# Optimization experiments

Measured on AMD Instinct MI355X. Metric: run time of the kernel, lower is better.

## Reference

```python
import jax, jax.numpy as jnp
import numpy as np

B, T, K = 64, 4096, 48  # batch, seq_len, n_tags


def setup_inputs() -> dict:
    key = jax.random.key(0)
    k1, k2, k3 = jax.random.split(key, 3)
    labels = jax.random.randint(k1, (B, T), 0, K)
    y_true = jax.nn.one_hot(labels, K, dtype=jnp.float32)  # one-hot targets, per dense_loss docstring
    y_pred = jax.random.normal(k2, (B, T, K), dtype=jnp.float32)  # emission scores
    trans = jax.random.normal(k3, (K, K), dtype=jnp.float32) * 0.1  # transition matrix (glorot-ish scale)
    return {"y_true": y_true, "y_pred": y_pred, "trans": trans}


def reference(y_true, y_pred, trans):
    # mask: positions where all emission scores > -1e6 (padding marker)
    mask = jnp.all(y_pred > -1e6, axis=2, keepdims=True).astype(y_pred.dtype)  # (B,T,1)
    y_true = y_true * mask
    y_pred = y_pred * mask

    # target_score: per-label emission score + transition score of the true path
    point_score = jnp.einsum('bni,bni->b', y_true, y_pred)
    trans_score = jnp.einsum('bni,ij,bnj->b', y_true[:, :-1], trans, y_true[:, 1:])
    target = point_score + trans_score  # (B,)

    # log_norm_step recurrence (CRF forward algorithm), fused as a single scan
    init = y_pred[:, 0]  # (B,K)
    xs = jnp.swapaxes(y_pred[:, 1:], 0, 1)  # (T-1,B,K)
    ms = jnp.swapaxes(mask[:, 1:], 0, 1)    # (T-1,B,1)

    def step(s, xm):
        x, m = xm
        # logsumexp over previous-tag axis: s (B,K_prev) + trans (K_prev,K_cur)
        new = jax.scipy.special.logsumexp(s[:, :, None] + trans[None, :, :], axis=1) + x
        s = m * new + (1.0 - m) * s
        return s, None

    s_final, _ = jax.lax.scan(step, init, (xs, ms))
    log_norm = jax.scipy.special.logsumexp(s_final, axis=1)  # (B,)

    # dense_loss returns log_norm - target_score (negative log-likelihood per example)
    return log_norm - target
```

## Files before the change

kernel.cpp:

```cpp
#include <hip/hip_runtime.h>

#define BB 64
#define TT 4096
#define KK 48
#define UST 56
#define PST 56
#define WS_LS_OFF 16384
#define WS_U_OFF 32768
#define SEGBYTES 6144

typedef __bf16 bf16_t;
typedef bf16_t bf16x8 __attribute__((ext_vector_type(8)));
typedef float f32x4 __attribute__((ext_vector_type(4)));
typedef float f32x16 __attribute__((ext_vector_type(16)));

__device__ __forceinline__ float fexp(float x) {
    return __builtin_amdgcn_exp2f(x * 1.4426950408889634f);
}
__device__ __forceinline__ float flog2(float x) { return __builtin_amdgcn_logf(x); }
__device__ __forceinline__ float rdlanef(float v, int l) {
    return __int_as_float(__builtin_amdgcn_readlane(__float_as_int(v), l));
}
__device__ __forceinline__ unsigned int bf16bits(float f) {
    return (unsigned int)__builtin_bit_cast(unsigned short, (bf16_t)f);
}
__device__ __forceinline__ float bf2f(bf16_t h) {
    return __uint_as_float(((unsigned int)__builtin_bit_cast(unsigned short, h)) << 16);
}
__device__ __forceinline__ unsigned int pktrunc(float lo, float hi) {
    return __builtin_amdgcn_perm(__float_as_uint(hi), __float_as_uint(lo), 0x07060302u);
}

__global__ __launch_bounds__(256) void fused_kernel(
    const float* __restrict__ y_true, const float* __restrict__ y_pred,
    const float* __restrict__ trans, float* __restrict__ ws_target,
    int* __restrict__ ws_ls, bf16_t* __restrict__ ws_u, int nseg) {
    const int s = blockIdx.x, b = blockIdx.y;
    const int seglen = TT / nseg;
    const int nch = seglen / 64;
    const int tid = threadIdx.x;
    const int w = tid >> 6;
    const int lane = tid & 63;
    const int q = lane >> 4;
    const int n = lane & 15;
    const int ncol = 16 * w + n;

    __shared__ __align__(16) float4 exf[64 * 13];
    __shared__ __align__(16) bf16_t Ubuf[48 * UST + 16];
    __shared__ unsigned long long pb;
    __shared__ int lsb[4];

    bf16x8 afrag[3][2];
    if (w < 3) {
#pragma unroll
        for (int mt = 0; mt < 3; mt++) {
#pragma unroll
            for (int ks = 0; ks < 2; ks++) {
                bf16x8 f;
#pragma unroll
                for (int j = 0; j < 8; j++) {
                    int k = 32 * ks + 8 * q + j;
                    float v = (k < KK) ? fexp(trans[k * KK + 16 * mt + n]) : 0.0f;
                    f[j] = (bf16_t)v;
                }
                afrag[mt][ks] = f;
            }
        }
    }

    {
        uint4* p = (uint4*)Ubuf;
        for (int i = tid; i < (48 * UST + 16) / 8; i += 256) p[i] = make_uint4(0, 0, 0, 0);
    }
    __syncthreads();
    if (tid < KK) Ubuf[tid * UST + tid] = (bf16_t)1.0f;

    const bf16_t* bptr0 = &Ubuf[ncol * UST + 8 * q];
    const bf16_t* bptr1 = &Ubuf[ncol * UST + 32 + 8 * q];
    bf16_t* wp0 = &Ubuf[ncol * UST + 0 + 4 * q];
    bf16_t* wp1 = &Ubuf[ncol * UST + 16 + 4 * q];
    bf16_t* wp2 = &Ubuf[ncol * UST + 32 + 4 * q];

    f32x4 z4 = {0.0f, 0.0f, 0.0f, 0.0f};
    int ls = 0;
    int cnt = 0;
    float sc_acc = 0.0f;

    for (int ch = 0; ch < nch; ch++) {
        __syncthreads();
        if (w == 3) {
            const int t0c = s * seglen + ch * 64;
            const size_t rowbase = ((size_t)b * TT + t0c + lane) * KK;
            const float4* yp4 = (const float4*)(y_pred + rowbase);
            const float4* yt4 = (const float4*)(y_true + rowbase);
            float dot = 0.0f, labf = 0.0f, pmin = 1e30f;
            float4* exrow = &exf[lane * 13];
#pragma unroll 4
            for (int g = 0; g < 12; g++) {
                float4 p = yp4[g];
                float4 a = yt4[g];
                dot = fmaf(a.x, p.x, fmaf(a.y, p.y, fmaf(a.z, p.z, fmaf(a.w, p.w, dot))));
                float e0 = (float)(4 * g);
                labf = fmaf(a.x, e0, fmaf(a.y, e0 + 1.0f, fmaf(a.z, e0 + 2.0f, fmaf(a.w, e0 + 3.0f, labf))));
                pmin = fminf(pmin, fminf(fminf(p.x, p.y), fminf(p.z, p.w)));
                exrow[g] = make_float4(fexp(p.x), fexp(p.y), fexp(p.z), fexp(p.w));
            }
            bool mt_ok = pmin > -1e6f;
            unsigned long long bal = __ballot(mt_ok);
            if (lane == 0) pb = bal;

            float labB = 0.0f, pmB = 1e30f;
            const bool hasB = (t0c + 64 < TT);
            if (hasB && lane < 12) {
                const size_t bdbase = ((size_t)b * TT + t0c + 64) * KK;
                float4 a = ((const float4*)(y_true + bdbase))[lane];
                float4 p = ((const float4*)(y_pred + bdbase))[lane];
                float e0 = (float)(4 * lane);
                labB = fmaf(a.x, e0, fmaf(a.y, e0 + 1.0f, fmaf(a.z, e0 + 2.0f, a.w * (e0 + 3.0f))));
                pmB = fminf(fminf(p.x, p.y), fminf(p.z, p.w));
            }
#pragma unroll
            for (int off = 1; off < 16; off <<= 1) {
                labB += __shfl_xor(labB, off);
                pmB = fminf(pmB, __shfl_xor(pmB, off));
            }
            int labB_i = (int)(rdlanef(labB, 0) + 0.5f);
            float mB = (hasB && rdlanef(pmB, 0) > -1e6f) ? 1.0f : 0.0f;

            int labt = (int)(labf + 0.5f);
            float mft = mt_ok ? 1.0f : 0.0f;
            int lnx = __shfl(labt, (lane + 1) & 63);
            float mnx = __shfl(mft, (lane + 1) & 63);
            if (lane == 63) { lnx = labB_i; mnx = mB; }
            sc_acc += mft * dot + mft * mnx * trans[labt * KK + lnx];
        }
        __syncthreads();
        if (w < 3) {
            const unsigned long long mk = pb;
            const int tt0 = (s == 0 && ch == 0) ? 1 : 0;
            for (int tt = tt0; tt < 64; tt++) {
                if (!((mk >> tt) & 1ull)) continue;

                bf16x8 bf0 = __builtin_bit_cast(bf16x8, *(const uint4*)bptr0);
                bf16x8 bf1 = __builtin_bit_cast(bf16x8, *(const uint4*)bptr1);

                f32x4 acc0 = __builtin_amdgcn_mfma_f32_16x16x32_bf16(afrag[0][0], bf0, z4, 0, 0, 0);
                acc0 = __builtin_amdgcn_mfma_f32_16x16x32_bf16(afrag[0][1], bf1, acc0, 0, 0, 0);
                f32x4 acc1 = __builtin_amdgcn_mfma_f32_16x16x32_bf16(afrag[1][0], bf0, z4, 0, 0, 0);
                acc1 = __builtin_amdgcn_mfma_f32_16x16x32_bf16(afrag[1][1], bf1, acc1, 0, 0, 0);
                f32x4 acc2 = __builtin_amdgcn_mfma_f32_16x16x32_bf16(afrag[2][0], bf0, z4, 0, 0, 0);
                acc2 = __builtin_amdgcn_mfma_f32_16x16x32_bf16(afrag[2][1], bf1, acc2, 0, 0, 0);

                float4 ex0 = exf[tt * 13 + q];
                float4 ex1 = exf[tt * 13 + 4 + q];
                float4 ex2 = exf[tt * 13 + 8 + q];

                if (++cnt >= 6) {
                    float v00 = rdlanef(acc0[0], 0);
                    int k = (int)(__float_as_uint(v00) >> 23) - 127;
                    float r = __uint_as_float((unsigned int)(127 - k) << 23);
                    ls += k;
                    ex0.x *= r; ex0.y *= r; ex0.z *= r; ex0.w *= r;
                    ex1.x *= r; ex1.y *= r; ex1.z *= r; ex1.w *= r;
                    ex2.x *= r; ex2.y *= r; ex2.z *= r; ex2.w *= r;
                    cnt = 0;
                }

                *(uint2*)wp0 = make_uint2(pktrunc(acc0[0] * ex0.x, acc0[1] * ex0.y),
                                          pktrunc(acc0[2] * ex0.z, acc0[3] * ex0.w));
                *(uint2*)wp1 = make_uint2(pktrunc(acc1[0] * ex1.x, acc1[1] * ex1.y),
                                          pktrunc(acc1[2] * ex1.z, acc1[3] * ex1.w));
                *(uint2*)wp2 = make_uint2(pktrunc(acc2[0] * ex2.x, acc2[1] * ex2.y),
                                          pktrunc(acc2[2] * ex2.z, acc2[3] * ex2.w));
            }
        }
    }

    if (w == 3) {
#pragma unroll
        for (int off = 32; off; off >>= 1) sc_acc += __shfl_xor(sc_acc, off);
        if (lane == 0) ws_target[b * nseg + s] = sc_acc;
    }

    if (w < 3 && lane == 0) lsb[w] = ls;
    __syncthreads();
    if (w < 3 && lane < KK) {
        const int dl = ls - lsb[0];
        bf16_t* Uo = ws_u + (size_t)(b * nseg + s) * 3072;
        unsigned int wd[8];
#pragma unroll
        for (int j = 0; j < 8; j++) {
            float f0 = ldexpf(bf2f(Ubuf[(16 * w + 2 * j) * UST + lane]), dl);
            float f1 = ldexpf(bf2f(Ubuf[(16 * w + 2 * j + 1) * UST + lane]), dl);
            wd[j] = bf16bits(f0) | (bf16bits(f1) << 16);
        }
        *(uint4*)(Uo + (size_t)lane * 64 + 16 * w) = make_uint4(wd[0], wd[1], wd[2], wd[3]);
        *(uint4*)(Uo + (size_t)lane * 64 + 16 * w + 8) = make_uint4(wd[4], wd[5], wd[6], wd[7]);
    }
    if (tid == 0) ws_ls[b * nseg + s] = lsb[0];
}

__device__ __forceinline__ int chain_product(const bf16_t* __restrict__ A, bf16_t* Ub, int lane) {
    const int half = lane >> 5;
    const int l31 = lane & 31;
    f32x16 z16;
#pragma unroll
    for (int r = 0; r < 16; r++) z16[r] = 0.0f;

    bf16x8 af[2][3];
#pragma unroll
    for (int mt = 0; mt < 2; mt++) {
        int m = l31 + 32 * mt;
#pragma unroll
        for (int ks = 0; ks < 3; ks++) {
            if (m < KK)
                af[mt][ks] = __builtin_bit_cast(bf16x8, *(const uint4*)&A[(size_t)m * 64 + 16 * ks + 8 * half]);
            else
                af[mt][ks] = __builtin_bit_cast(bf16x8, make_uint4(0, 0, 0, 0));
        }
    }
    bf16x8 bg[3][2];
#pragma unroll
    for (int ks = 0; ks < 3; ks++)
#pragma unroll
        for (int nt = 0; nt < 2; nt++)
            bg[ks][nt] = __builtin_bit_cast(bf16x8, *(const uint4*)&Ub[(l31 + 32 * nt) * PST + 16 * ks + 8 * half]);

    f32x16 acc[4];
#pragma unroll
    for (int mt = 0; mt < 2; mt++)
#pragma unroll
        for (int nt = 0; nt < 2; nt++) {
            f32x16 a0 = __builtin_amdgcn_mfma_f32_32x32x16_bf16(af[mt][0], bg[0][nt], z16, 0, 0, 0);
            a0 = __builtin_amdgcn_mfma_f32_32x32x16_bf16(af[mt][1], bg[1][nt], a0, 0, 0, 0);
            acc[mt * 2 + nt] = __builtin_amdgcn_mfma_f32_32x32x16_bf16(af[mt][2], bg[2][nt], a0, 0, 0, 0);
        }

    float v00 = rdlanef(acc[0][0], 0);
    int k = (int)(__float_as_uint(v00) >> 23) - 127;
    float r = __uint_as_float((unsigned int)(127 - k) << 23);

#pragma unroll
    for (int mt = 0; mt < 2; mt++)
#pragma unroll
        for (int nt = 0; nt < 2; nt++) {
            int c = l31 + 32 * nt;
#pragma unroll
            for (int g = 0; g < 4; g++) {
                int a0 = 32 * mt + 8 * g + 4 * half;
                if (a0 < KK) {
                    const f32x16& Aq = acc[mt * 2 + nt];
                    unsigned int u0 = bf16bits(Aq[4 * g + 0] * r) | (bf16bits(Aq[4 * g + 1] * r) << 16);
                    unsigned int u1 = bf16bits(Aq[4 * g + 2] * r) | (bf16bits(Aq[4 * g + 3] * r) << 16);
                    *(uint2*)&Ub[c * PST + a0] = make_uint2(u0, u1);
                }
            }
        }
    return k;
}

__device__ __forceinline__ int chain_product_ldsA(const bf16_t* As, bf16_t* Ub, int lane) {
    const int half = lane >> 5;
    const int l31 = lane & 31;
    f32x16 z16;
#pragma unroll
    for (int r = 0; r < 16; r++) z16[r] = 0.0f;

    bf16x8 af[2][3];
#pragma unroll
    for (int mt = 0; mt < 2; mt++) {
        int m = l31 + 32 * mt;
#pragma unroll
        for (int ks = 0; ks < 3; ks++) {
            bf16x8 f;
#pragma unroll
            for (int j = 0; j < 8; j++) {
                int k = 16 * ks + 8 * half + j;
                f[j] = (m < KK) ? As[k * PST + m] : (bf16_t)0.0f;
            }
            af[mt][ks] = f;
        }
    }
    bf16x8 bg[3][2];
#pragma unroll
    for (int ks = 0; ks < 3; ks++)
#pragma unroll
        for (int nt = 0; nt < 2; nt++)
            bg[ks][nt] = __builtin_bit_cast(bf16x8, *(const uint4*)&Ub[(l31 + 32 * nt) * PST + 16 * ks + 8 * half]);

    f32x16 acc[4];
#pragma unroll
    for (int mt = 0; mt < 2; mt++)
#pragma unroll
        for (int nt = 0; nt < 2; nt++) {
            f32x16 a0 = __builtin_amdgcn_mfma_f32_32x32x16_bf16(af[mt][0], bg[0][nt], z16, 0, 0, 0);
            a0 = __builtin_amdgcn_mfma_f32_32x32x16_bf16(af[mt][1], bg[1][nt], a0, 0, 0, 0);
            acc[mt * 2 + nt] = __builtin_amdgcn_mfma_f32_32x32x16_bf16(af[mt][2], bg[2][nt], a0, 0, 0, 0);
        }

    float v00 = rdlanef(acc[0][0], 0);
    int k = (int)(__float_as_uint(v00) >> 23) - 127;
    float r = __uint_as_float((unsigned int)(127 - k) << 23);

#pragma unroll
    for (int mt = 0; mt < 2; mt++)
#pragma unroll
        for (int nt = 0; nt < 2; nt++) {
            int c = l31 + 32 * nt;
#pragma unroll
            for (int g = 0; g < 4; g++) {
                int a0 = 32 * mt + 8 * g + 4 * half;
                if (a0 < KK) {
                    const f32x16& Aq = acc[mt * 2 + nt];
                    unsigned int u0 = bf16bits(Aq[4 * g + 0] * r) | (bf16bits(Aq[4 * g + 1] * r) << 16);
                    unsigned int u1 = bf16bits(Aq[4 * g + 2] * r) | (bf16bits(Aq[4 * g + 3] * r) << 16);
                    *(uint2*)&Ub[c * PST + a0] = make_uint2(u0, u1);
                }
            }
        }
    return k;
}

__global__ __launch_bounds__(256) void phaseAB_kernel(
    const float* __restrict__ y_pred, const bf16_t* __restrict__ ws_u,
    const int* __restrict__ ws_ls, const float* __restrict__ ws_target,
    float* __restrict__ out, int nseg) {
    const int b = blockIdx.x;
    const int tid = threadIdx.x;
    const int w = tid >> 6;
    const int lane = tid & 63;
    const int per = nseg / 4;

    __shared__ __align__(16) bf16_t Ws[4][64 * PST];
    __shared__ int lsw[4];

    const int base = b * nseg + w * per;
    const bf16_t* s0 = ws_u + (size_t)base * 3072;
    for (int k = 0; k < KK; k++)
        Ws[w][lane * PST + k] = (lane < KK) ? s0[(size_t)k * 64 + lane] : (bf16_t)0.0f;
    int lsk = ws_ls[base];
    for (int j = 1; j < per; j++) {
        const bf16_t* A = ws_u + (size_t)(base + j) * 3072;
        lsk += ws_ls[base + j];
        lsk += chain_product(A, Ws[w], lane);
    }
    if (lane == 0) lsw[w] = lsk;
    __syncthreads();

    if (w == 0) {
        int ls2 = 0;
#pragma unroll
        for (int j = 1; j < 4; j++) ls2 += chain_product_ldsA(Ws[j], Ws[0], lane);

        float L = (float)(lsw[0] + lsw[1] + lsw[2] + lsw[3] + ls2);

        float x0 = (lane < KK) ? y_pred[(size_t)b * TT * KK + lane] : 0.0f;
        bool ok0 = (lane >= KK) || (x0 > -1e6f);
        bool m0 = (__ballot(ok0) == ~0ull);
        float xeff = (lane < KK) ? (m0 ? x0 : 0.0f) : 0.0f;
        float c0 = rdlanef(xeff, 0);
        float q0 = (lane < KK) ? fexp(xeff - c0) : 0.0f;

        float p = 0.0f;
        if (lane < KK) {
            for (int c = 0; c < KK; c++) {
                float qc = rdlanef(q0, c);
                p = fmaf(bf2f(Ws[0][c * PST + lane]), qc, p);
            }
        }
#pragma unroll
        for (int off = 32; off; off >>= 1) p += __shfl_xor(p, off);

        float tg = (lane < nseg) ? ws_target[b * nseg + lane] : 0.0f;
#pragma unroll
        for (int off = 32; off; off >>= 1) tg += __shfl_xor(tg, off);

        if (lane == 0) {
            out[b] = c0 + 0.6931471805599453f * (L + flog2(p)) - tg;
        }
    }
}

extern "C" void kernel_launch(void* const* d_in, const int* in_sizes, int n_in,
                              void* d_out, int out_size, void* d_ws, size_t ws_size,
                              hipStream_t stream) {
    const float* y_true = (const float*)d_in[0];
    const float* y_pred = (const float*)d_in[1];
    const float* trans = (const float*)d_in[2];
    float* out = (float*)d_out;

    int nseg = 16;
    if (ws_size >= (size_t)WS_U_OFF + (size_t)BB * 64 * SEGBYTES) nseg = 64;
    else if (ws_size >= (size_t)WS_U_OFF + (size_t)BB * 32 * SEGBYTES) nseg = 32;

    float* ws_target = (float*)d_ws;
    int* ws_ls = (int*)((char*)d_ws + WS_LS_OFF);
    bf16_t* ws_u = (bf16_t*)((char*)d_ws + WS_U_OFF);

    fused_kernel<<<dim3(nseg, BB), 256, 0, stream>>>(
        y_true, y_pred, trans, ws_target, ws_ls, ws_u, nseg);
    phaseAB_kernel<<<BB, 256, 0, stream>>>(y_pred, ws_u, ws_ls, ws_target, out, nseg);
}
```

Before: 269.2 us.

## Double-buffer emission staging, compact segment matrices, tree-fold final products, cap segments

The producer warp now prepares the next 64-step chunk into a second LDS buffer while the three MFMA warps run the recurrence on the current one, which removes one barrier per chunk. Per-segment transfer matrices are stored with a 48-element row stride instead of 64, shrinking workspace traffic. The final fold combines the four partial products as a two-level tree instead of three sequential products. The segment count is capped at 32 instead of 64, and launch bounds request 4 blocks per CU. The exponential loads are restructured into the rescale branch. Fewer segments lengthen each block's serial chain, and the doubled LDS buffer may limit occupancy.

```diff
diff --git a/kernel.cpp b/kernel.cpp
--- a/kernel.cpp
+++ b/kernel.cpp
@@ -7,7 +7,8 @@
 #define PST 56
 #define WS_LS_OFF 16384
 #define WS_U_OFF 32768
-#define SEGBYTES 6144
+#define SEGBYTES 4608
+#define SEGELEMS 2304
 
 typedef __bf16 bf16_t;
 typedef bf16_t bf16x8 __attribute__((ext_vector_type(8)));
@@ -31,7 +32,7 @@
     return __builtin_amdgcn_perm(__float_as_uint(hi), __float_as_uint(lo), 0x07060302u);
 }
 
-__global__ __launch_bounds__(256) void fused_kernel(
+__global__ __launch_bounds__(256, 4) void fused_kernel(
     const float* __restrict__ y_true, const float* __restrict__ y_pred,
     const float* __restrict__ trans, float* __restrict__ ws_target,
     int* __restrict__ ws_ls, bf16_t* __restrict__ ws_u, int nseg) {
@@ -45,9 +46,9 @@
     const int n = lane & 15;
     const int ncol = 16 * w + n;
 
-    __shared__ __align__(16) float4 exf[64 * 13];
+    __shared__ __align__(16) float4 exf[2][64 * 13];
     __shared__ __align__(16) bf16_t Ubuf[48 * UST + 16];
-    __shared__ unsigned long long pb;
+    __shared__ unsigned long long pbb[2];
     __shared__ int lsb[4];
 
     bf16x8 afrag[3][2];
@@ -86,57 +87,62 @@
     int cnt = 0;
     float sc_acc = 0.0f;
 
+    auto produce = [&](int ch, int buf) {
+        const int t0c = s * seglen + ch * 64;
+        const size_t rowbase = ((size_t)b * TT + t0c + lane) * KK;
+        const float4* yp4 = (const float4*)(y_pred + rowbase);
+        const float4* yt4 = (const float4*)(y_true + rowbase);
+        float dot = 0.0f, labf = 0.0f, pmin = 1e30f;
+        float4* exrow = &exf[buf][lane * 13];
+#pragma unroll 4
+        for (int g = 0; g < 12; g++) {
+            float4 p = yp4[g];
+            float4 a = yt4[g];
+            dot = fmaf(a.x, p.x, fmaf(a.y, p.y, fmaf(a.z, p.z, fmaf(a.w, p.w, dot))));
+            float e0 = (float)(4 * g);
+            labf = fmaf(a.x, e0, fmaf(a.y, e0 + 1.0f, fmaf(a.z, e0 + 2.0f, fmaf(a.w, e0 + 3.0f, labf))));
+            pmin = fminf(pmin, fminf(fminf(p.x, p.y), fminf(p.z, p.w)));
+            exrow[g] = make_float4(fexp(p.x), fexp(p.y), fexp(p.z), fexp(p.w));
+        }
+        bool mt_ok = pmin > -1e6f;
+        unsigned long long bal = __ballot(mt_ok);
+        if (lane == 0) pbb[buf] = bal;
+
+        float labB = 0.0f, pmB = 1e30f;
+        const bool hasB = (t0c + 64 < TT);
+        if (hasB && lane < 12) {
+            const size_t bdbase = ((size_t)b * TT + t0c + 64) * KK;
+            float4 a = ((const float4*)(y_true + bdbase))[lane];
+            float4 p = ((const float4*)(y_pred + bdbase))[lane];
+            float e0 = (float)(4 * lane);
+            labB = fmaf(a.x, e0, fmaf(a.y, e0 + 1.0f, fmaf(a.z, e0 + 2.0f, a.w * (e0 + 3.0f))));
+            pmB = fminf(fminf(p.x, p.y), fminf(p.z, p.w));
+        }
+#pragma unroll
+        for (int off = 1; off < 16; off <<= 1) {
+            labB += __shfl_xor(labB, off);
+            pmB = fminf(pmB, __shfl_xor(pmB, off));
+        }
+        int labB_i = (int)(rdlanef(labB, 0) + 0.5f);
+        float mB = (hasB && rdlanef(pmB, 0) > -1e6f) ? 1.0f : 0.0f;
+
+        int labt = (int)(labf + 0.5f);
+        float mft = mt_ok ? 1.0f : 0.0f;
+        int lnx = __shfl(labt, (lane + 1) & 63);
+        float mnx = __shfl(mft, (lane + 1) & 63);
+        if (lane == 63) { lnx = labB_i; mnx = mB; }
+        sc_acc += mft * dot + mft * mnx * trans[labt * KK + lnx];
+    };
+
+    if (w == 3) produce(0, 0);
+    __syncthreads();
+
     for (int ch = 0; ch < nch; ch++) {
-        __syncthreads();
+        const int cur = ch & 1;
         if (w == 3) {
-            const int t0c = s * seglen + ch * 64;
-            const size_t rowbase = ((size_t)b * TT + t0c + lane) * KK;
-            const float4* yp4 = (const float4*)(y_pred + rowbase);
-            const float4* yt4 = (const float4*)(y_true + rowbase);
-            float dot = 0.0f, labf = 0.0f, pmin = 1e30f;
-            float4* exrow = &exf[lane * 13];
-#pragma unroll 4
-            for (int g = 0; g < 12; g++) {
-                float4 p = yp4[g];
-                float4 a = yt4[g];
-                dot = fmaf(a.x, p.x, fmaf(a.y, p.y, fmaf(a.z, p.z, fmaf(a.w, p.w, dot))));
-                float e0 = (float)(4 * g);
-                labf = fmaf(a.x, e0, fmaf(a.y, e0 + 1.0f, fmaf(a.z, e0 + 2.0f, fmaf(a.w, e0 + 3.0f, labf))));
-                pmin = fminf(pmin, fminf(fminf(p.x, p.y), fminf(p.z, p.w)));
-                exrow[g] = make_float4(fexp(p.x), fexp(p.y), fexp(p.z), fexp(p.w));
-            }
-            bool mt_ok = pmin > -1e6f;
-            unsigned long long bal = __ballot(mt_ok);
-            if (lane == 0) pb = bal;
-
-            float labB = 0.0f, pmB = 1e30f;
-            const bool hasB = (t0c + 64 < TT);
-            if (hasB && lane < 12) {
-                const size_t bdbase = ((size_t)b * TT + t0c + 64) * KK;
-                float4 a = ((const float4*)(y_true + bdbase))[lane];
-                float4 p = ((const float4*)(y_pred + bdbase))[lane];
-                float e0 = (float)(4 * lane);
-                labB = fmaf(a.x, e0, fmaf(a.y, e0 + 1.0f, fmaf(a.z, e0 + 2.0f, a.w * (e0 + 3.0f))));
-                pmB = fminf(fminf(p.x, p.y), fminf(p.z, p.w));
-            }
-#pragma unroll
-            for (int off = 1; off < 16; off <<= 1) {
-                labB += __shfl_xor(labB, off);
-                pmB = fminf(pmB, __shfl_xor(pmB, off));
-            }
-            int labB_i = (int)(rdlanef(labB, 0) + 0.5f);
-            float mB = (hasB && rdlanef(pmB, 0) > -1e6f) ? 1.0f : 0.0f;
-
-            int labt = (int)(labf + 0.5f);
-            float mft = mt_ok ? 1.0f : 0.0f;
-            int lnx = __shfl(labt, (lane + 1) & 63);
-            float mnx = __shfl(mft, (lane + 1) & 63);
-            if (lane == 63) { lnx = labB_i; mnx = mB; }
-            sc_acc += mft * dot + mft * mnx * trans[labt * KK + lnx];
-        }
-        __syncthreads();
-        if (w < 3) {
-            const unsigned long long mk = pb;
+            if (ch + 1 < nch) produce(ch + 1, cur ^ 1);
+        } else {
+            const unsigned long long mk = pbb[cur];
             const int tt0 = (s == 0 && ch == 0) ? 1 : 0;
             for (int tt = tt0; tt < 64; tt++) {
                 if (!((mk >> tt) & 1ull)) continue;
@@ -151,29 +157,38 @@
                 f32x4 acc2 = __builtin_amdgcn_mfma_f32_16x16x32_bf16(afrag[2][0], bf0, z4, 0, 0, 0);
                 acc2 = __builtin_amdgcn_mfma_f32_16x16x32_bf16(afrag[2][1], bf1, acc2, 0, 0, 0);
 
-                float4 ex0 = exf[tt * 13 + q];
-                float4 ex1 = exf[tt * 13 + 4 + q];
-                float4 ex2 = exf[tt * 13 + 8 + q];
-
                 if (++cnt >= 6) {
                     float v00 = rdlanef(acc0[0], 0);
                     int k = (int)(__float_as_uint(v00) >> 23) - 127;
                     float r = __uint_as_float((unsigned int)(127 - k) << 23);
                     ls += k;
+                    cnt = 0;
+                    float4 ex0 = exf[cur][tt * 13 + q];
                     ex0.x *= r; ex0.y *= r; ex0.z *= r; ex0.w *= r;
+                    *(uint2*)wp0 = make_uint2(pktrunc(acc0[0] * ex0.x, acc0[1] * ex0.y),
+                                              pktrunc(acc0[2] * ex0.z, acc0[3] * ex0.w));
+                    float4 ex1 = exf[cur][tt * 13 + 4 + q];
                     ex1.x *= r; ex1.y *= r; ex1.z *= r; ex1.w *= r;
+                    *(uint2*)wp1 = make_uint2(pktrunc(acc1[0] * ex1.x, acc1[1] * ex1.y),
+                                              pktrunc(acc1[2] * ex1.z, acc1[3] * ex1.w));
+                    float4 ex2 = exf[cur][tt * 13 + 8 + q];
                     ex2.x *= r; ex2.y *= r; ex2.z *= r; ex2.w *= r;
-                    cnt = 0;
+                    *(uint2*)wp2 = make_uint2(pktrunc(acc2[0] * ex2.x, acc2[1] * ex2.y),
+                                              pktrunc(acc2[2] * ex2.z, acc2[3] * ex2.w));
+                } else {
+                    float4 ex0 = exf[cur][tt * 13 + q];
+                    *(uint2*)wp0 = make_uint2(pktrunc(acc0[0] * ex0.x, acc0[1] * ex0.y),
+                                              pktrunc(acc0[2] * ex0.z, acc0[3] * ex0.w));
+                    float4 ex1 = exf[cur][tt * 13 + 4 + q];
+                    *(uint2*)wp1 = make_uint2(pktrunc(acc1[0] * ex1.x, acc1[1] * ex1.y),
+                                              pktrunc(acc1[2] * ex1.z, acc1[3] * ex1.w));
+                    float4 ex2 = exf[cur][tt * 13 + 8 + q];
+                    *(uint2*)wp2 = make_uint2(pktrunc(acc2[0] * ex2.x, acc2[1] * ex2.y),
+                                              pktrunc(acc2[2] * ex2.z, acc2[3] * ex2.w));
                 }
-
-                *(uint2*)wp0 = make_uint2(pktrunc(acc0[0] * ex0.x, acc0[1] * ex0.y),
-                                          pktrunc(acc0[2] * ex0.z, acc0[3] * ex0.w));
-                *(uint2*)wp1 = make_uint2(pktrunc(acc1[0] * ex1.x, acc1[1] * ex1.y),
-                                          pktrunc(acc1[2] * ex1.z, acc1[3] * ex1.w));
-                *(uint2*)wp2 = make_uint2(pktrunc(acc2[0] * ex2.x, acc2[1] * ex2.y),
-                                          pktrunc(acc2[2] * ex2.z, acc2[3] * ex2.w));
-            }
-        }
+            }
+        }
+        __syncthreads();
     }
 
     if (w == 3) {
@@ -186,7 +201,7 @@
     __syncthreads();
     if (w < 3 && lane < KK) {
         const int dl = ls - lsb[0];
-        bf16_t* Uo = ws_u + (size_t)(b * nseg + s) * 3072;
+        bf16_t* Uo = ws_u + (size_t)(b * nseg + s) * SEGELEMS;
         unsigned int wd[8];
 #pragma unroll
         for (int j = 0; j < 8; j++) {
@@ -194,8 +209,8 @@
             float f1 = ldexpf(bf2f(Ubuf[(16 * w + 2 * j + 1) * UST + lane]), dl);
             wd[j] = bf16bits(f0) | (bf16bits(f1) << 16);
         }
-        *(uint4*)(Uo + (size_t)lane * 64 + 16 * w) = make_uint4(wd[0], wd[1], wd[2], wd[3]);
-        *(uint4*)(Uo + (size_t)lane * 64 + 16 * w + 8) = make_uint4(wd[4], wd[5], wd[6], wd[7]);
+        *(uint4*)(Uo + (size_t)lane * 48 + 16 * w) = make_uint4(wd[0], wd[1], wd[2], wd[3]);
+        *(uint4*)(Uo + (size_t)lane * 48 + 16 * w + 8) = make_uint4(wd[4], wd[5], wd[6], wd[7]);
     }
     if (tid == 0) ws_ls[b * nseg + s] = lsb[0];
 }
@@ -214,7 +229,7 @@
 #pragma unroll
         for (int ks = 0; ks < 3; ks++) {
             if (m < KK)
-                af[mt][ks] = __builtin_bit_cast(bf16x8, *(const uint4*)&A[(size_t)m * 64 + 16 * ks + 8 * half]);
+                af[mt][ks] = __builtin_bit_cast(bf16x8, *(const uint4*)&A[(size_t)m * 48 + 16 * ks + 8 * half]);
             else
                 af[mt][ks] = __builtin_bit_cast(bf16x8, make_uint4(0, 0, 0, 0));
         }
@@ -321,38 +336,44 @@
     return k;
 }
 
-__global__ __launch_bounds__(256) void phaseAB_kernel(
+__global__ __launch_bounds__(256) void fold_final_kernel(
     const float* __restrict__ y_pred, const bf16_t* __restrict__ ws_u,
     const int* __restrict__ ws_ls, const float* __restrict__ ws_target,
     float* __restrict__ out, int nseg) {
     const int b = blockIdx.x;
     const int tid = threadIdx.x;
-    const int w = tid >> 6;
-    const int lane = tid & 63;
+    const int w = tid >> 6, lane = tid & 63;
     const int per = nseg / 4;
 
     __shared__ __align__(16) bf16_t Ws[4][64 * PST];
-    __shared__ int lsw[4];
-
-    const int base = b * nseg + w * per;
-    const bf16_t* s0 = ws_u + (size_t)base * 3072;
-    for (int k = 0; k < KK; k++)
-        Ws[w][lane * PST + k] = (lane < KK) ? s0[(size_t)k * 64 + lane] : (bf16_t)0.0f;
-    int lsk = ws_ls[base];
-    for (int j = 1; j < per; j++) {
-        const bf16_t* A = ws_u + (size_t)(base + j) * 3072;
-        lsk += ws_ls[base + j];
-        lsk += chain_product(A, Ws[w], lane);
-    }
-    if (lane == 0) lsw[w] = lsk;
+    __shared__ int lsp[8];
+    if (tid < 8) lsp[tid] = 0;
+    __syncthreads();
+
+    {
+        const int base = b * nseg + per * w;
+        const bf16_t* s0 = ws_u + (size_t)base * SEGELEMS;
+        for (int k = 0; k < KK; k++)
+            Ws[w][lane * PST + k] = (lane < KK) ? s0[(size_t)k * 48 + lane] : (bf16_t)0.0f;
+        int lsk = ws_ls[base];
+        for (int j = 1; j < per; j++) {
+            lsk += ws_ls[base + j];
+            lsk += chain_product(ws_u + (size_t)(base + j) * SEGELEMS, Ws[w], lane);
+        }
+        if (lane == 0) lsp[w] = lsk;
+    }
+    __syncthreads();
+    int k1 = 0;
+    if (w == 0) k1 = chain_product_ldsA(Ws[1], Ws[0], lane);
+    if (w == 2) {
+        int k2 = chain_product_ldsA(Ws[3], Ws[2], lane);
+        if (lane == 0) lsp[5] = k2;
+    }
     __syncthreads();
 
     if (w == 0) {
-        int ls2 = 0;
-#pragma unroll
-        for (int j = 1; j < 4; j++) ls2 += chain_product_ldsA(Ws[j], Ws[0], lane);
-
-        float L = (float)(lsw[0] + lsw[1] + lsw[2] + lsw[3] + ls2);
+        int k3 = chain_product_ldsA(Ws[2], Ws[0], lane);
+        float L = (float)(lsp[0] + lsp[1] + lsp[2] + lsp[3] + k1 + lsp[5] + k3);
 
         float x0 = (lane < KK) ? y_pred[(size_t)b * TT * KK + lane] : 0.0f;
         bool ok0 = (lane >= KK) || (x0 > -1e6f);
@@ -390,8 +411,7 @@
     float* out = (float*)d_out;
 
     int nseg = 16;
-    if (ws_size >= (size_t)WS_U_OFF + (size_t)BB * 64 * SEGBYTES) nseg = 64;
-    else if (ws_size >= (size_t)WS_U_OFF + (size_t)BB * 32 * SEGBYTES) nseg = 32;
+    if (ws_size >= (size_t)WS_U_OFF + (size_t)BB * 32 * SEGBYTES) nseg = 32;
 
     float* ws_target = (float*)d_ws;
     int* ws_ls = (int*)((char*)d_ws + WS_LS_OFF);
@@ -399,5 +419,5 @@
 
     fused_kernel<<<dim3(nseg, BB), 256, 0, stream>>>(
         y_true, y_pred, trans, ws_target, ws_ls, ws_u, nseg);
-    phaseAB_kernel<<<BB, 256, 0, stream>>>(y_pred, ws_u, ws_ls, ws_target, out, nseg);
-}
+    fold_final_kernel<<<BB, 256, 0, stream>>>(y_pred, ws_u, ws_ls, ws_target, out, nseg);
+}
```

New measurement: 235.7 us. 1.14x faster.
